# Performance work log

Hardware: AMD Instinct MI355X
Metric: run time of the kernel (lower is better)

## Reference

```python
import jax, jax.numpy as jnp
import numpy as np

INPUT_DIM = 256
OUTPUT_DIM = 16
MAX_HIDDEN = 768
NUM_NODES = INPUT_DIM + OUTPUT_DIM + MAX_HIDDEN          # 1040
NUM_MIDDLE = OUTPUT_DIM + MAX_HIDDEN                     # 784
BATCH = 32768


def setup_inputs() -> dict:
    key = jax.random.key(0)
    k1, k2, k3, k4 = jax.random.split(key, 4)
    x = jax.random.normal(k1, (BATCH, INPUT_DIM), dtype=jnp.float32)
    weight = jax.random.normal(k2, (NUM_NODES, NUM_MIDDLE), dtype=jnp.float32) * 0.1
    bias = jax.random.normal(k3, (NUM_MIDDLE,), dtype=jnp.float32) * 0.1
    connectivity = jax.random.randint(k4, (NUM_NODES, NUM_MIDDLE), 0, 2, dtype=jnp.int32)
    node_existence = jnp.ones((NUM_MIDDLE,), dtype=jnp.int32)
    return {
        "x": x,
        "weight": weight,
        "bias": bias,
        "connectivity": connectivity,
        "node_existence": node_existence,
        "output_dim": OUTPUT_DIM,
    }


def reference(x, weight, bias, connectivity, node_existence, output_dim):
    B = x.shape[0]
    N, M = weight.shape                 # num_nodes, num_middle_result_nodes
    input_dim = N - M
    eff = weight * connectivity.astype(weight.dtype)   # [N, M] masked weights
    ex = node_existence.astype(weight.dtype)           # [M]
    results0 = jnp.zeros((B, N), dtype=x.dtype).at[:, :input_dim].set(x)
    node_idx = jnp.arange(N)

    def step(results, i):
        # only nodes < input_dim + i feed node i (faithful to growing slice)
        valid = (node_idx < input_dim + i).astype(eff.dtype)   # [N]
        w_col = jnp.take(eff, i, axis=1) * valid               # [N]
        res = results @ w_col                                   # [B]
        res = (jax.nn.sigmoid(res) + bias[i]) * ex[i]
        results = jax.lax.dynamic_update_slice(results, res[:, None], (0, input_dim + i))
        return results, None

    results, _ = jax.lax.scan(step, results0, jnp.arange(M))
    return results[:, -output_dim:]
```

## Files before the change

### kernel.cpp

```cpp
#include <hip/hip_runtime.h>
#include <cstdint>
#include <cstddef>

#define INPUT_DIM 256
#define OUT_DIM   16
#define NMID      784
#define NNODE     1040
#define KPAD      1056
#define KB        16
#define NBLK      49
#define NCHMAX    32
#define LROW      1032

typedef float f32x4 __attribute__((ext_vector_type(4)));
typedef __bf16 bf16x8 __attribute__((ext_vector_type(8)));

#define GLL16(gp, lp)                                                        \
  __builtin_amdgcn_global_load_lds(                                          \
      (const __attribute__((address_space(1))) unsigned int*)(gp),           \
      (__attribute__((address_space(3))) unsigned int*)(lp), 16, 0, 0)

static __device__ __forceinline__ unsigned int f2bf(float f) {
  unsigned int u = __builtin_bit_cast(unsigned int, f);
  u += 0x7fffu + ((u >> 16) & 1u);
  return u >> 16;
}
static __device__ __forceinline__ float bf2f(unsigned short h) {
  unsigned int u = ((unsigned int)h) << 16;
  return __builtin_bit_cast(float, u);
}

__global__ __launch_bounds__(256) void prep_efft(
    const float* __restrict__ w, const int* __restrict__ conn,
    const int* __restrict__ ex, unsigned short* __restrict__ effT) {
  __shared__ unsigned short tile[64][66];
  const int j0 = blockIdx.x * 64;
  const int i0 = blockIdx.y * 64;
  const int tx = threadIdx.x & 63;
  const int ty = threadIdx.x >> 6;
  const int i  = i0 + tx;
  for (int t = 0; t < 16; ++t) {
    int j = j0 + t * 4 + ty;
    float v = 0.f;
    if (j < NNODE && i < NMID && j < INPUT_DIM + i) {
      float e = (j >= INPUT_DIM) ? (float)ex[j - INPUT_DIM] : 1.f;
      v = w[(size_t)j * NMID + i] * (float)conn[(size_t)j * NMID + i] * e;
    }
    tile[t * 4 + ty][tx] = (unsigned short)f2bf(v);
  }
  __syncthreads();
  const int i_loc = threadIdx.x >> 2;
  const int jq    = threadIdx.x & 3;
  const int iw    = i0 + i_loc;
  const int jbase = j0 + jq * 16;
  if (iw < NMID && jbase + 16 <= KPAD) {
    #pragma unroll
    for (int c = 0; c < 16; ++c)
      effT[(size_t)iw * KPAD + jbase + c] = tile[jq * 16 + c][i_loc];
  }
}

__global__ __launch_bounds__(64) void prep_cvec(
    const unsigned short* __restrict__ effT, const float* __restrict__ bias,
    float* __restrict__ cvec) {
  const int i = blockIdx.x;
  const int l = threadIdx.x;
  float s = 0.f;
  for (int jj = l; jj < NMID; jj += 64)
    s += bf2f(effT[(size_t)i * KPAD + INPUT_DIM + jj]) * bias[jj];
  for (int off = 32; off; off >>= 1) s += __shfl_down(s, off, 64);
  if (l == 0) cvec[i] = s;
}

__global__ __launch_bounds__(256) void prep_wpack(
    const float* __restrict__ w, const int* __restrict__ conn,
    const int* __restrict__ ex, float* __restrict__ wpack) {
  const int b = blockIdx.x;
  const int k = threadIdx.x >> 4;
  const int c = threadIdx.x & 15;
  const int src = KB * b + k;
  const int dst = KB * b + c;
  float v = 0.f;
  if (k < c) {
    size_t idx = (size_t)(INPUT_DIM + src) * NMID + dst;
    v = w[idx] * (float)conn[idx] * (float)ex[src];
  }
  wpack[b * 256 + k * 16 + c] = v;
}

__global__ __launch_bounds__(256, 2) void net_main(
    const float* __restrict__ x, const unsigned short* __restrict__ effT,
    const float* __restrict__ cvec, const float* __restrict__ wpack,
    const float* __restrict__ bias, const int* __restrict__ ex,
    float* __restrict__ out) {
  __shared__ unsigned short Bs[2][16 * LROW];
  __shared__ float wtri2[2][256];
  __shared__ float scrS[4][320];

  const int tid = threadIdx.x;
  const int l   = tid & 63;
  const int wv  = tid >> 6;
  const int g   = l >> 4;
  const int r16 = l & 15;
  const int grow = (blockIdx.x * 4 + wv) * 16 + r16;

  float* myscr = scrS[wv];

  uint4 sfrag[NCHMAX];
  #pragma unroll
  for (int c = 0; c < 8; ++c) {
    const float* p = x + (size_t)grow * INPUT_DIM + 32 * c + 8 * g;
    float4 v0 = *(const float4*)p;
    float4 v1 = *(const float4*)(p + 4);
    uint4 u;
    u.x = f2bf(v0.x) | (f2bf(v0.y) << 16);
    u.y = f2bf(v0.z) | (f2bf(v0.w) << 16);
    u.z = f2bf(v1.x) | (f2bf(v1.y) << 16);
    u.w = f2bf(v1.z) | (f2bf(v1.w) << 16);
    sfrag[c] = u;
  }
  #pragma unroll
  for (int c = 8; c < NCHMAX; ++c) {
    uint4 z; z.x = z.y = z.z = z.w = 0u;
    sfrag[c] = z;
  }

#define STAGE_B(nb, t)                                                        \
  {                                                                           \
    _Pragma("unroll")                                                         \
    for (int k_ = 0; k_ < 4; ++k_) {                                          \
      const int r_ = 4 * wv + k_;                                             \
      const char* gsrc_ =                                                     \
          (const char*)(effT + (size_t)(16 * (t) + r_) * KPAD) + l * 16;      \
      unsigned short* ldst_ = &Bs[nb][r_ * LROW];                             \
      GLL16(gsrc_, ldst_);                                                    \
      GLL16(gsrc_ + 1024, (char*)ldst_ + 1024);                               \
    }                                                                         \
  }
#define STAGE_W(nb, t)                                                        \
  if (l < 16) {                                                               \
    *(float4*)&wtri2[nb][wv * 64 + 4 * l] =                                   \
        *(const float4*)&wpack[(t) * 256 + wv * 64 + 4 * l];                  \
  }

  STAGE_B(0, 0);
  STAGE_W(0, 0);
  __syncthreads();

  for (int b = 0; b < NBLK; ++b) {
    const int cur = b & 1;

    if (b + 1 < NBLK) {
      STAGE_B(cur ^ 1, b + 1);
      STAGE_W(cur ^ 1, b + 1);
    }

    f32x4 ac0 = {0.f,0.f,0.f,0.f}, ac1 = ac0, ac2 = ac0, ac3 = ac0;
    const unsigned short* bb = &Bs[cur][r16 * LROW + g * 8];
#define CHUNK(c)                                                              \
  {                                                                           \
    uint4 braw = *(const uint4*)(bb + (c) * 32);                              \
    f32x4& a_ = ((c) & 3) == 0 ? ac0 : ((c) & 3) == 1 ? ac1                   \
               : ((c) & 3) == 2 ? ac2 : ac3;                                  \
    a_ = __builtin_amdgcn_mfma_f32_16x16x32_bf16(                             \
        __builtin_bit_cast(bf16x8, sfrag[(c)]),                               \
        __builtin_bit_cast(bf16x8, braw), a_, 0, 0, 0);                       \
  }
    CHUNK(0) CHUNK(1) CHUNK(2) CHUNK(3) CHUNK(4) CHUNK(5) CHUNK(6) CHUNK(7)
    if (b >= 1) {
      CHUNK(8) CHUNK(9) CHUNK(10) CHUNK(11)
      CHUNK(12) CHUNK(13) CHUNK(14) CHUNK(15)
    }
    if (b >= 17) {
      CHUNK(16) CHUNK(17) CHUNK(18) CHUNK(19)
      CHUNK(20) CHUNK(21) CHUNK(22) CHUNK(23)
    }
    if (b >= 33) {
      CHUNK(24) CHUNK(25) CHUNK(26) CHUNK(27)
      CHUNK(28) CHUNK(29) CHUNK(30) CHUNK(31)
    }
#undef CHUNK
    f32x4 accsum = (ac0 + ac1) + (ac2 + ac3);

    #pragma unroll
    for (int i = 0; i < 4; ++i)
      myscr[(4 * g + i) * 20 + r16] = accsum[i];
    float acc_t[16];
    #pragma unroll
    for (int c = 0; c < 16; ++c)
      acc_t[c] = myscr[r16 * 20 + c];

    const float* wtri = wtri2[cur];
    #pragma unroll
    for (int k = 0; k < 16; ++k) {
      float xk = acc_t[k] + cvec[KB * b + k];
      float s  = __builtin_amdgcn_rcpf(
          1.f + __builtin_amdgcn_exp2f(xk * -1.44269504088896341f));
      acc_t[k] = s;
      const float4* wrow = (const float4*)(wtri + k * 16);
      float4 w0 = wrow[0], w1 = wrow[1], w2 = wrow[2], w3 = wrow[3];
      float wr[16] = {w0.x, w0.y, w0.z, w0.w, w1.x, w1.y, w1.z, w1.w,
                      w2.x, w2.y, w2.z, w2.w, w3.x, w3.y, w3.z, w3.w};
      #pragma unroll
      for (int c = k + 1; c < 16; ++c) acc_t[c] += s * wr[c];
    }

    if (b == NBLK - 1) {
      #pragma unroll
      for (int i = 0; i < 4; ++i) {
        int oc = 4 * g + i;
        int mi = NMID - OUT_DIM + oc;
        out[(size_t)grow * OUT_DIM + oc] =
            (acc_t[oc] + bias[mi]) * (float)ex[mi];
      }
    } else {
      const int cw = 8 + (b >> 1);
      const int vb = 8 * (g & 1);
      uint4 packed;
      packed.x = f2bf(acc_t[vb + 0]) | (f2bf(acc_t[vb + 1]) << 16);
      packed.y = f2bf(acc_t[vb + 2]) | (f2bf(acc_t[vb + 3]) << 16);
      packed.z = f2bf(acc_t[vb + 4]) | (f2bf(acc_t[vb + 5]) << 16);
      packed.w = f2bf(acc_t[vb + 6]) | (f2bf(acc_t[vb + 7]) << 16);
      const bool part = ((g >> 1) == (b & 1));
      #pragma unroll
      for (int c = 8; c < NCHMAX; ++c) {
        if (c == cw) {
          if (part) sfrag[c] = packed;
        }
      }
    }

    __syncthreads();
  }
#undef STAGE_B
#undef STAGE_W
}

extern "C" void kernel_launch(void* const* d_in, const int* in_sizes, int n_in,
                              void* d_out, int out_size, void* d_ws, size_t ws_size,
                              hipStream_t stream) {
  const float* x      = (const float*)d_in[0];
  const float* weight = (const float*)d_in[1];
  const float* bias   = (const float*)d_in[2];
  const int*   conn   = (const int*)d_in[3];
  const int*   ex     = (const int*)d_in[4];

  unsigned short* effT = (unsigned short*)d_ws;
  float* cvec  = (float*)((char*)d_ws + (size_t)NMID * KPAD * 2);
  float* wpack = (float*)((char*)d_ws + (size_t)NMID * KPAD * 2 + NMID * 4);

  prep_efft<<<dim3(17, 13), 256, 0, stream>>>(weight, conn, ex, effT);
  prep_cvec<<<dim3(NMID), 64, 0, stream>>>(effT, bias, cvec);
  prep_wpack<<<dim3(NBLK), 256, 0, stream>>>(weight, conn, ex, wpack);
  net_main<<<dim3(32768 / 64), 256, 0, stream>>>(
      x, effT, cvec, wpack, bias, ex, (float*)d_out);
}
```

Measured before the change: 223.9 us.

## Read triangular weights directly from global as scalars, fold cvec into diagonal, repad LDS rows

Removes the per-block LDS staging of the 16x16 triangular weight block and instead reads wpack straight from global memory with wave-uniform addresses, which the compiler can turn into scalar loads. The cvec offset is folded into the diagonal of wpack so one buffer serves both. The LDS row pitch for the staged effT tile is changed from 1032 to 1064 elements, meant to change bank mapping for the MFMA B reads. The trade is extra scalar-memory latency on the serial sigmoid chain in exchange for less LDS traffic and fewer vector instructions.

Result: slower. 349.2 us (+56.0%).

```diff
diff --git a/kernel.cpp b/kernel.cpp
--- a/kernel.cpp
+++ b/kernel.cpp
@@ -10,7 +10,7 @@
 #define KB        16
 #define NBLK      49
 #define NCHMAX    32
-#define LROW      1032
+#define LROW      1064
 
 typedef float f32x4 __attribute__((ext_vector_type(4)));
 typedef __bf16 bf16x8 __attribute__((ext_vector_type(8)));
@@ -74,7 +74,8 @@
 
 __global__ __launch_bounds__(256) void prep_wpack(
     const float* __restrict__ w, const int* __restrict__ conn,
-    const int* __restrict__ ex, float* __restrict__ wpack) {
+    const int* __restrict__ ex, const float* __restrict__ cvec,
+    float* __restrict__ wpack) {
   const int b = blockIdx.x;
   const int k = threadIdx.x >> 4;
   const int c = threadIdx.x & 15;
@@ -84,17 +85,17 @@
   if (k < c) {
     size_t idx = (size_t)(INPUT_DIM + src) * NMID + dst;
     v = w[idx] * (float)conn[idx] * (float)ex[src];
+  } else if (k == c) {
+    v = cvec[src];
   }
   wpack[b * 256 + k * 16 + c] = v;
 }
 
 __global__ __launch_bounds__(256, 2) void net_main(
     const float* __restrict__ x, const unsigned short* __restrict__ effT,
-    const float* __restrict__ cvec, const float* __restrict__ wpack,
-    const float* __restrict__ bias, const int* __restrict__ ex,
-    float* __restrict__ out) {
-  __shared__ unsigned short Bs[2][16 * LROW];
-  __shared__ float wtri2[2][256];
+    const float* __restrict__ wpack, const float* __restrict__ bias,
+    const int* __restrict__ ex, float* __restrict__ out) {
+  __shared__ __align__(16) unsigned short Bs[2][16 * LROW];
   __shared__ float scrS[4][320];
 
   const int tid = threadIdx.x;
@@ -137,14 +138,8 @@
       GLL16(gsrc_ + 1024, (char*)ldst_ + 1024);                               \
     }                                                                         \
   }
-#define STAGE_W(nb, t)                                                        \
-  if (l < 16) {                                                               \
-    *(float4*)&wtri2[nb][wv * 64 + 4 * l] =                                   \
-        *(const float4*)&wpack[(t) * 256 + wv * 64 + 4 * l];                  \
-  }
 
   STAGE_B(0, 0);
-  STAGE_W(0, 0);
   __syncthreads();
 
   for (int b = 0; b < NBLK; ++b) {
@@ -152,7 +147,6 @@
 
     if (b + 1 < NBLK) {
       STAGE_B(cur ^ 1, b + 1);
-      STAGE_W(cur ^ 1, b + 1);
     }
 
     f32x4 ac0 = {0.f,0.f,0.f,0.f}, ac1 = ac0, ac2 = ac0, ac3 = ac0;
@@ -190,19 +184,16 @@
     for (int c = 0; c < 16; ++c)
       acc_t[c] = myscr[r16 * 20 + c];
 
-    const float* wtri = wtri2[cur];
+    const float* wp = wpack + b * 256;
     #pragma unroll
     for (int k = 0; k < 16; ++k) {
-      float xk = acc_t[k] + cvec[KB * b + k];
+      float xk = acc_t[k] + wp[k * 16 + k];
       float s  = __builtin_amdgcn_rcpf(
           1.f + __builtin_amdgcn_exp2f(xk * -1.44269504088896341f));
       acc_t[k] = s;
-      const float4* wrow = (const float4*)(wtri + k * 16);
-      float4 w0 = wrow[0], w1 = wrow[1], w2 = wrow[2], w3 = wrow[3];
-      float wr[16] = {w0.x, w0.y, w0.z, w0.w, w1.x, w1.y, w1.z, w1.w,
-                      w2.x, w2.y, w2.z, w2.w, w3.x, w3.y, w3.z, w3.w};
       #pragma unroll
-      for (int c = k + 1; c < 16; ++c) acc_t[c] += s * wr[c];
+      for (int c = k + 1; c < 16; ++c)
+        acc_t[c] = __builtin_fmaf(s, wp[k * 16 + c], acc_t[c]);
     }
 
     if (b == NBLK - 1) {
@@ -233,7 +224,6 @@
     __syncthreads();
   }
 #undef STAGE_B
-#undef STAGE_W
 }
 
 extern "C" void kernel_launch(void* const* d_in, const int* in_sizes, int n_in,
@@ -251,7 +241,7 @@
 
   prep_efft<<<dim3(17, 13), 256, 0, stream>>>(weight, conn, ex, effT);
   prep_cvec<<<dim3(NMID), 64, 0, stream>>>(effT, bias, cvec);
-  prep_wpack<<<dim3(NBLK), 256, 0, stream>>>(weight, conn, ex, wpack);
+  prep_wpack<<<dim3(NBLK), 256, 0, stream>>>(weight, conn, ex, cvec, wpack);
   net_main<<<dim3(32768 / 64), 256, 0, stream>>>(
-      x, effT, cvec, wpack, bias, ex, (float*)d_out);
-}
+      x, effT, wpack, bias, ex, (float*)d_out);
+}
```
